# Kernel optimization log

Measured on AMD Instinct MI355X. Metric: run time of the kernel, lower is better.

Reference implementation:

```python
import jax, jax.numpy as jnp
import numpy as np


def _phi(x):
    # ELU(x) + 1 feature map (positive kernel feature map)
    return jax.nn.elu(x) + 1.0


def setup_inputs() -> dict:
    key = jax.random.key(0)
    k1, k2, k3 = jax.random.split(key, 3)
    B, S, E = 4, 4096, 1024
    inputs = jax.random.normal(k1, (B, S, E), dtype=jnp.float32)
    mask = jnp.ones((B, S), dtype=jnp.float32)
    w_qkv = jax.random.normal(k2, (3 * E, E), dtype=jnp.float32) * (E ** -0.5)
    b_qkv = jax.random.normal(k3, (3 * E,), dtype=jnp.float32) * 0.02
    return {"inputs": inputs, "mask": mask, "w_qkv": w_qkv, "b_qkv": b_qkv, "num_heads": 16}


def reference(inputs, mask, w_qkv, b_qkv, num_heads):
    B, S, E = inputs.shape
    H = num_heads
    D = E // H
    # qkv projection: torch Linear is x @ W.T + b
    qkv = inputs @ w_qkv.T + b_qkv                     # (B, S, 3E)
    qkv = qkv.reshape(B, S, 3, H, D)
    q = qkv[:, :, 0]                                   # (B, S, H, D)
    k = qkv[:, :, 1]
    v = qkv[:, :, 2]
    # key masking (float multiply, as in einsum 'bshd,bs->bshd')
    k = k * mask[:, :, None, None]
    kq = _phi(q)                                       # (B, S, H, D)
    kk = _phi(k)                                       # (B, S, H, D)
    # kv outer-product accumulation over sequence: (B, H, M, D)
    kv = jnp.einsum('bshd,bshm->bhmd', kk, v)
    # normalizer
    z = 1.0 / (jnp.einsum('bshd,bhd->bsh', kq, kk.sum(axis=1)) + 1e-6)
    # final contraction
    attn = jnp.einsum('bshd,bhmd,bsh->bshm', kq, kv, z)  # (B, S, H, D)
    attn = attn.reshape(B, S, E)
    # NOTE: original forward computes a projection but returns `attn` (dropout is
    # identity at inference), so projection is dead code and omitted here.
    return attn
```

## Files before the change

kernel.cpp:

```cpp
#include <hip/hip_runtime.h>

typedef unsigned short u16;
typedef short bf16x8 __attribute__((ext_vector_type(8)));
typedef float f32x4 __attribute__((ext_vector_type(4)));
typedef u16 u16x8 __attribute__((ext_vector_type(8)));
typedef u16 u16x4 __attribute__((ext_vector_type(4)));

#define B_ 4
#define S_ 4096
#define E_ 1024
#define H_ 16
#define D_ 64
#define M_ 16384
#define N_ 3072
#define K_ 1024

__device__ __forceinline__ u16 f2b(float f) {
    unsigned x = __builtin_bit_cast(unsigned, f);
    return (u16)((x + 0x7fffu + ((x >> 16) & 1u)) >> 16);
}
__device__ __forceinline__ float b2f(u16 u) {
    unsigned x = ((unsigned)u) << 16;
    return __builtin_bit_cast(float, x);
}
__device__ __forceinline__ float phi_f(float x) { return x > 0.f ? x + 1.f : __expf(x); }

__device__ __forceinline__ void gload16(const void* g, void* l) {
    __builtin_amdgcn_global_load_lds((const __attribute__((address_space(1))) void*)g,
                                     (__attribute__((address_space(3))) void*)l, 16, 0, 0);
}

#define MEMFENCE asm volatile("" ::: "memory")

__global__ void cvt_bf16(const float* __restrict__ in, u16* __restrict__ out, int n8) {
    int stride = gridDim.x * blockDim.x;
    for (int i = blockIdx.x * blockDim.x + threadIdx.x; i < n8; i += stride) {
        const float4* p = (const float4*)(in + (size_t)i * 8);
        float4 a = p[0], b = p[1];
        u16x8 o;
        o[0] = f2b(a.x); o[1] = f2b(a.y); o[2] = f2b(a.z); o[3] = f2b(a.w);
        o[4] = f2b(b.x); o[5] = f2b(b.y); o[6] = f2b(b.z); o[7] = f2b(b.w);
        *(u16x8*)(out + (size_t)i * 8) = o;
    }
}


__global__ __launch_bounds__(512, 2) void gemm_qkv(
    const u16* __restrict__ Abf, const u16* __restrict__ Wbf,
    const float* __restrict__ bias, const float* __restrict__ mask,
    u16* __restrict__ KQ, u16* __restrict__ KKT, u16* __restrict__ VT)
{
    __shared__ __align__(16) char lds[131072];

    int wg  = blockIdx.x;
    int xcd = wg & 7, ii = wg >> 3;
    int tm  = xcd * 8 + ii / 12;
    int tn  = ii % 12;
    int m0 = tm << 8, n0 = tn << 8;

    int t = threadIdx.x;
    int l = t & 63, wid = t >> 6;
    int wr = wid >> 2, wc = wid & 3;
    int lg = l >> 4, lr = l & 15;

    int srow  = t >> 3;
    int scolE = ((t & 7) ^ (srow & 7)) << 3;
    int t16   = t * 16;

    const u16* gA = Abf + (size_t)(m0 + srow) * K_ + scolE;
    const u16* gB = Wbf + (size_t)(n0 + srow) * K_ + scolE;

    const char* aB = lds + (wr * 128 + lr) * 128;
    const char* bB = lds + 32768 + (wc * 64 + lr) * 128;
    int pc0 = (lg * 16) ^ ((lr & 7) << 4);
    int pc1 = pc0 ^ 64;

    f32x4 acc[8][4] = {};
    bf16x8 av[4][2], b01[2][2], b23[2][2];

#define RD_A(BO, MI0) { _Pragma("unroll") for (int m_ = 0; m_ < 4; ++m_) { \
    av[m_][0] = *(const bf16x8*)(aB + (BO) + (MI0 + m_) * 2048 + pc0); \
    av[m_][1] = *(const bf16x8*)(aB + (BO) + (MI0 + m_) * 2048 + pc1); } }

#define RD_B01(BO) { _Pragma("unroll") for (int n_ = 0; n_ < 2; ++n_) { \
    b01[n_][0] = *(const bf16x8*)(bB + (BO) + n_ * 2048 + pc0); \
    b01[n_][1] = *(const bf16x8*)(bB + (BO) + n_ * 2048 + pc1); } }

#define RD_B23(BO) { _Pragma("unroll") for (int n_ = 0; n_ < 2; ++n_) { \
    b23[n_][0] = *(const bf16x8*)(bB + (BO) + (2 + n_) * 2048 + pc0); \
    b23[n_][1] = *(const bf16x8*)(bB + (BO) + (2 + n_) * 2048 + pc1); } }

#define ST_A(TT, HI, BO) { \
    gload16(gA + (size_t)((HI) * 64) * K_ + (TT) * 64, lds + (BO) + (HI) * 8192 + t16); \
    gload16(gA + (size_t)((HI) * 64 + 128) * K_ + (TT) * 64, lds + (BO) + 16384 + (HI) * 8192 + t16); }

#define ST_B(TT, PR, BO) { \
    gload16(gB + (size_t)((PR) * 128) * K_ + (TT) * 64, lds + (BO) + 32768 + (PR) * 16384 + t16); \
    gload16(gB + (size_t)((PR) * 128 + 64) * K_ + (TT) * 64, lds + (BO) + 32768 + (PR) * 16384 + 8192 + t16); }

#define BAR { MEMFENCE; __builtin_amdgcn_s_barrier(); MEMFENCE; }
#define LGKM0 { asm volatile("s_waitcnt lgkmcnt(0)" ::: "memory"); \
                __builtin_amdgcn_sched_barrier(0); }

#define MM16(MI0, NI0, BV) { __builtin_amdgcn_s_setprio(1); \
    _Pragma("unroll") for (int m_ = 0; m_ < 4; ++m_) \
    _Pragma("unroll") for (int n_ = 0; n_ < 2; ++n_) \
    _Pragma("unroll") for (int h_ = 0; h_ < 2; ++h_) \
        acc[(MI0) + m_][(NI0) + n_] = __builtin_amdgcn_mfma_f32_16x16x32_bf16( \
            av[m_][h_], BV[n_][h_], acc[(MI0) + m_][(NI0) + n_], 0, 0, 0); \
    __builtin_amdgcn_s_setprio(0); }

    ST_A(0, 0, 0); ST_B(0, 0, 0); ST_B(0, 1, 0); ST_A(0, 1, 0);
    ST_A(1, 0, 65536); ST_B(1, 0, 65536);
    asm volatile("s_waitcnt vmcnt(4)" ::: "memory");
    __builtin_amdgcn_s_barrier();
    MEMFENCE;

#pragma unroll 1
    for (int kt = 0; kt < 16; kt += 2) {
        int tp2 = kt + 2 < 16 ? kt + 2 : 15;
        int tp3 = kt + 3 < 16 ? kt + 3 : 15;
        RD_A(0, 0); RD_B01(0); ST_A(kt + 1, 1, 65536);
        BAR; LGKM0; MM16(0, 0, b01);
        RD_B23(0); ST_B(kt + 1, 1, 65536);
        BAR; LGKM0; MM16(0, 2, b23);
        RD_A(0, 4); ST_A(tp2, 0, 0);
        BAR; LGKM0; MM16(4, 2, b23);
        ST_B(tp2, 0, 0);
        asm volatile("s_waitcnt vmcnt(4)" ::: "memory");
        BAR; LGKM0; MM16(4, 0, b01);
        RD_A(65536, 0); RD_B01(65536); ST_A(tp2, 1, 0);
        BAR; LGKM0; MM16(0, 0, b01);
        RD_B23(65536); ST_B(tp2, 1, 0);
        BAR; LGKM0; MM16(0, 2, b23);
        RD_A(65536, 4); ST_A(tp3, 0, 65536);
        BAR; LGKM0; MM16(4, 2, b23);
        ST_B(tp3, 0, 65536);
        asm volatile("s_waitcnt vmcnt(4)" ::: "memory");
        BAR; LGKM0; MM16(4, 0, b01);
    }

    int part = n0 >> 10;

    float bv[4];
#pragma unroll
    for (int ni = 0; ni < 4; ++ni) bv[ni] = bias[n0 + wc * 64 + ni * 16 + lr];

    if (part == 0) {
#pragma unroll
        for (int mi = 0; mi < 8; ++mi)
#pragma unroll
            for (int j = 0; j < 4; ++j) {
                int row = m0 + wr * 128 + mi * 16 + lg * 4 + j;
#pragma unroll
                for (int ni = 0; ni < 4; ++ni) {
                    int col = n0 + wc * 64 + ni * 16 + lr;
                    KQ[(size_t)row * E_ + col] = f2b(phi_f(acc[mi][ni][j] + bv[ni]));
                }
            }
    } else {
        u16* dst0 = (part == 1) ? KKT : VT;
        int b  = m0 >> 12;
        int sl = m0 & (S_ - 1);
        int h  = ((tn & 3) << 2) | wc;
#pragma unroll
        for (int mi = 0; mi < 8; ++mi) {
            int sbase = sl + wr * 128 + mi * 16 + lg * 4;
            float mk[4];
#pragma unroll
            for (int j = 0; j < 4; ++j)
                mk[j] = (part == 1) ? mask[m0 + wr * 128 + mi * 16 + lg * 4 + j] : 1.f;
#pragma unroll
            for (int ni = 0; ni < 4; ++ni) {
                u16x4 o;
#pragma unroll
                for (int j = 0; j < 4; ++j) {
                    float v = acc[mi][ni][j] + bv[ni];
                    if (part == 1) v = phi_f(v * mk[j]);
                    o[j] = f2b(v);
                }
                int d = ni * 16 + lr;
                *(u16x4*)(dst0 + ((size_t)((b * H_ + h) * D_ + d)) * S_ + sbase) = o;
            }
        }
    }
}

__global__ __launch_bounds__(256) void kv_ksum_partial(
    const u16* __restrict__ VT, const u16* __restrict__ KKT,
    float* __restrict__ KVP, float* __restrict__ KSP)
{
    __shared__ __align__(16) u16 smem[8192];
    u16* As = smem;
    u16* Bs = smem + 4096;
    int bh = blockIdx.x;
    int ch = blockIdx.y;
    int s0 = ch << 8;
    int t = threadIdx.x;
    int l = t & 63, w = t >> 6;
    int lg = l >> 4, lr = l & 15;
    const u16* Ag = VT + (size_t)bh * (D_ * S_);
    const u16* Bg = KKT + (size_t)bh * (D_ * S_);
    int srow = t >> 3, scol = (t & 7) << 3;

    f32x4 acc[4] = {};
    float ks = 0.f;
    int kd = t >> 2;
    int kq4 = (t & 3) << 4;

    for (int kt = 0; kt < 4; ++kt) {
        __syncthreads();
        int sb = s0 + kt * 64;
#pragma unroll
        for (int i = 0; i < 2; ++i) {
            gload16(Ag + (size_t)(srow + i * 32) * S_ + sb + scol, As + i * 2048 + t * 8);
            gload16(Bg + (size_t)(srow + i * 32) * S_ + sb + scol, Bs + i * 2048 + t * 8);
        }
        __syncthreads();
#pragma unroll
        for (int i = 0; i < 16; ++i) ks += b2f(Bs[kd * 64 + kq4 + i]);
#pragma unroll
        for (int kh = 0; kh < 2; ++kh) {
            int ko = kh * 32 + lg * 8;
            bf16x8 a = *(const bf16x8*)&As[(w * 16 + lr) * 64 + ko];
#pragma unroll
            for (int ni = 0; ni < 4; ++ni) {
                bf16x8 bb = *(const bf16x8*)&Bs[(ni * 16 + lr) * 64 + ko];
                acc[ni] = __builtin_amdgcn_mfma_f32_16x16x32_bf16(a, bb, acc[ni], 0, 0, 0);
            }
        }
    }
    float* kvp = KVP + (size_t)ch * (64 * 4096) + bh * 4096;
#pragma unroll
    for (int ni = 0; ni < 4; ++ni)
#pragma unroll
        for (int j = 0; j < 4; ++j)
            kvp[(w * 16 + lg * 4 + j) * 64 + ni * 16 + lr] = acc[ni][j];
    ks += __shfl_xor(ks, 1);
    ks += __shfl_xor(ks, 2);
    if ((t & 3) == 0) KSP[ch * 4096 + bh * 64 + kd] = ks;
}

__global__ void reduce_kv(const float* __restrict__ KVP, const float* __restrict__ KSP,
                          float* __restrict__ KV, float* __restrict__ KSUM)
{
    int g = blockIdx.x * 256 + threadIdx.x;
#pragma unroll 1
    for (int i = g * 4; i < g * 4 + 4; ++i) {
        float s = 0.f;
#pragma unroll
        for (int c = 0; c < 16; ++c) s += KVP[(size_t)c * (64 * 4096) + i];
        KV[i] = s;
    }
    if (g < 4096) {
        float s = 0.f;
#pragma unroll
        for (int c = 0; c < 16; ++c) s += KSP[c * 4096 + g];
        KSUM[g] = s;
    }
}

__global__ __launch_bounds__(256) void attn_out(
    const u16* __restrict__ KQ, const float* __restrict__ KV,
    const float* __restrict__ KSUM, float* __restrict__ Out)
{
    __shared__ __align__(16) u16 kqs[16384];
    __shared__ __align__(16) u16 bsm[5120];
    __shared__ float den[256];
    int bh = blockIdx.x, ch = blockIdx.y;
    int b = bh >> 4, h = bh & 15;
    int t = threadIdx.x;
    int l = t & 63, w = t >> 6;
    int lg = l >> 4, lr = l & 15;
    size_t row0 = (size_t)b * S_ + ch * 256;
    int srow = t >> 3, scol = (t & 7) << 3;
#pragma unroll
    for (int i = 0; i < 8; ++i)
        gload16(KQ + (row0 + srow + i * 32) * E_ + h * 64 + scol, kqs + i * 2048 + t * 8);

    const float* kvg = KV + bh * 4096;
#pragma unroll
    for (int ii = 0; ii < 16; ii += 4) {
        float4 v = *(const float4*)(kvg + t * 16 + ii);
        u16x4 o; o[0] = f2b(v.x); o[1] = f2b(v.y); o[2] = f2b(v.z); o[3] = f2b(v.w);
        *(u16x4*)&bsm[t * 16 + ii] = o;
    }
    if (t < 64) bsm[4096 + t] = f2b(KSUM[bh * 64 + t]);
    for (int i = t; i < 960; i += 256) bsm[4160 + i] = 0;
    __syncthreads();

    f32x4 acc[4][5] = {};
#pragma unroll
    for (int kh = 0; kh < 2; ++kh) {
        int ko = kh * 32 + lg * 8;
        bf16x8 af[4];
#pragma unroll
        for (int mi = 0; mi < 4; ++mi)
            af[mi] = *(const bf16x8*)&kqs[(w * 64 + mi * 16 + lr) * 64 + ko];
#pragma unroll
        for (int ni = 0; ni < 5; ++ni) {
            bf16x8 bb = *(const bf16x8*)&bsm[(ni * 16 + lr) * 64 + ko];
#pragma unroll
            for (int mi = 0; mi < 4; ++mi)
                acc[mi][ni] = __builtin_amdgcn_mfma_f32_16x16x32_bf16(af[mi], bb, acc[mi][ni], 0, 0, 0);
        }
    }
    if (lr == 0) {
#pragma unroll
        for (int mi = 0; mi < 4; ++mi)
#pragma unroll
            for (int j = 0; j < 4; ++j)
                den[w * 64 + mi * 16 + lg * 4 + j] = acc[mi][4][j];
    }
    __syncthreads();
#pragma unroll
    for (int mi = 0; mi < 4; ++mi)
#pragma unroll
        for (int j = 0; j < 4; ++j) {
            int sl = w * 64 + mi * 16 + lg * 4 + j;
            float z = 1.f / (den[sl] + 1e-6f);
            float* op = Out + (row0 + sl) * E_ + h * 64;
#pragma unroll
            for (int ni = 0; ni < 4; ++ni)
                op[ni * 16 + lr] = acc[mi][ni][j] * z;
        }
}

extern "C" void kernel_launch(void* const* d_in, const int* in_sizes, int n_in,
                              void* d_out, int out_size, void* d_ws, size_t ws_size,
                              hipStream_t stream)
{
    const float* inputs = (const float*)d_in[0];
    const float* mask   = (const float*)d_in[1];
    const float* w_qkv  = (const float*)d_in[2];
    const float* b_qkv  = (const float*)d_in[3];

    u16* Abf = (u16*)d_ws;
    u16* Wbf = Abf + (size_t)M_ * K_;
    u16* KQ  = Wbf + (size_t)N_ * K_;
    float* KVP  = (float*)(KQ + (size_t)M_ * E_);
    float* KSP  = KVP + 16 * 64 * 4096;
    float* KV   = KSP + 16 * 4096;
    float* KSUM = KV + 64 * 4096;

    u16* KKT = (u16*)d_out;
    u16* VT  = KKT + (size_t)M_ * E_;

    cvt_bf16<<<2048, 256, 0, stream>>>(inputs, Abf, M_ * K_ / 8);
    cvt_bf16<<<768, 256, 0, stream>>>(w_qkv, Wbf, N_ * K_ / 8);
    gemm_qkv<<<768, 512, 0, stream>>>(Abf, Wbf, b_qkv, mask, KQ, KKT, VT);
    kv_ksum_partial<<<dim3(64, 16), 256, 0, stream>>>(VT, KKT, KVP, KSP);
    reduce_kv<<<256, 256, 0, stream>>>(KVP, KSP, KV, KSUM);
    attn_out<<<dim3(64, 16), 256, 0, stream>>>(KQ, KV, KSUM, (float*)d_out);
}
```

Measured before the change: 171.9 us.

## Fuse KV/ksum partial reduction into QKV GEMM, keeping phi(K) in LDS

Each workgroup now computes the V, K and Q tiles for one 256-row block and four heads in sequence. The phi(K) tile is written transposed into LDS instead of to global memory, and the V^T·phi(K) partial product and the key-sum partial are computed in the same kernel. This removes the separate kv_ksum_partial launch and the global round trip of the K^T buffer. In exchange the grid shrinks from 768 to 256 workgroups of three serial tiles each, which lowers parallelism on a machine with many CUs. V is also re-read from global memory immediately after it is written.

```diff
diff --git a/kernel.cpp b/kernel.cpp
--- a/kernel.cpp
+++ b/kernel.cpp
@@ -31,6 +31,10 @@
 }
 
 #define MEMFENCE asm volatile("" ::: "memory")
+#define BAR { MEMFENCE; __builtin_amdgcn_s_barrier(); MEMFENCE; }
+#define LGKM0 { asm volatile("s_waitcnt lgkmcnt(0)" ::: "memory"); \
+                __builtin_amdgcn_sched_barrier(0); }
+#define VMCNT(n) asm volatile("s_waitcnt vmcnt(" #n ")" ::: "memory")
 
 __global__ void cvt_bf16(const float* __restrict__ in, u16* __restrict__ out, int n8) {
     int stride = gridDim.x * blockDim.x;
@@ -45,39 +49,6 @@
 }
 
 
-__global__ __launch_bounds__(512, 2) void gemm_qkv(
-    const u16* __restrict__ Abf, const u16* __restrict__ Wbf,
-    const float* __restrict__ bias, const float* __restrict__ mask,
-    u16* __restrict__ KQ, u16* __restrict__ KKT, u16* __restrict__ VT)
-{
-    __shared__ __align__(16) char lds[131072];
-
-    int wg  = blockIdx.x;
-    int xcd = wg & 7, ii = wg >> 3;
-    int tm  = xcd * 8 + ii / 12;
-    int tn  = ii % 12;
-    int m0 = tm << 8, n0 = tn << 8;
-
-    int t = threadIdx.x;
-    int l = t & 63, wid = t >> 6;
-    int wr = wid >> 2, wc = wid & 3;
-    int lg = l >> 4, lr = l & 15;
-
-    int srow  = t >> 3;
-    int scolE = ((t & 7) ^ (srow & 7)) << 3;
-    int t16   = t * 16;
-
-    const u16* gA = Abf + (size_t)(m0 + srow) * K_ + scolE;
-    const u16* gB = Wbf + (size_t)(n0 + srow) * K_ + scolE;
-
-    const char* aB = lds + (wr * 128 + lr) * 128;
-    const char* bB = lds + 32768 + (wc * 64 + lr) * 128;
-    int pc0 = (lg * 16) ^ ((lr & 7) << 4);
-    int pc1 = pc0 ^ 64;
-
-    f32x4 acc[8][4] = {};
-    bf16x8 av[4][2], b01[2][2], b23[2][2];
-
 #define RD_A(BO, MI0) { _Pragma("unroll") for (int m_ = 0; m_ < 4; ++m_) { \
     av[m_][0] = *(const bf16x8*)(aB + (BO) + (MI0 + m_) * 2048 + pc0); \
     av[m_][1] = *(const bf16x8*)(aB + (BO) + (MI0 + m_) * 2048 + pc1); } }
@@ -97,10 +68,6 @@
 #define ST_B(TT, PR, BO) { \
     gload16(gB + (size_t)((PR) * 128) * K_ + (TT) * 64, lds + (BO) + 32768 + (PR) * 16384 + t16); \
     gload16(gB + (size_t)((PR) * 128 + 64) * K_ + (TT) * 64, lds + (BO) + 32768 + (PR) * 16384 + 8192 + t16); }
-
-#define BAR { MEMFENCE; __builtin_amdgcn_s_barrier(); MEMFENCE; }
-#define LGKM0 { asm volatile("s_waitcnt lgkmcnt(0)" ::: "memory"); \
-                __builtin_amdgcn_sched_barrier(0); }
 
 #define MM16(MI0, NI0, BV) { __builtin_amdgcn_s_setprio(1); \
     _Pragma("unroll") for (int m_ = 0; m_ < 4; ++m_) \
@@ -110,43 +77,165 @@
             av[m_][h_], BV[n_][h_], acc[(MI0) + m_][(NI0) + n_], 0, 0, 0); \
     __builtin_amdgcn_s_setprio(0); }
 
+__device__ __forceinline__ void run_tile(
+    const u16* gA, const u16* gB, char* lds, int t16,
+    const char* aB, const char* bB, int pc0, int pc1, f32x4 (&acc)[8][4])
+{
+    bf16x8 av[4][2], b01[2][2], b23[2][2];
     ST_A(0, 0, 0); ST_B(0, 0, 0); ST_B(0, 1, 0); ST_A(0, 1, 0);
     ST_A(1, 0, 65536); ST_B(1, 0, 65536);
-    asm volatile("s_waitcnt vmcnt(4)" ::: "memory");
+    VMCNT(4);
     __builtin_amdgcn_s_barrier();
     MEMFENCE;
-
 #pragma unroll 1
     for (int kt = 0; kt < 16; kt += 2) {
         int tp2 = kt + 2 < 16 ? kt + 2 : 15;
         int tp3 = kt + 3 < 16 ? kt + 3 : 15;
-        RD_A(0, 0); RD_B01(0); ST_A(kt + 1, 1, 65536);
-        BAR; LGKM0; MM16(0, 0, b01);
-        RD_B23(0); ST_B(kt + 1, 1, 65536);
-        BAR; LGKM0; MM16(0, 2, b23);
-        RD_A(0, 4); ST_A(tp2, 0, 0);
-        BAR; LGKM0; MM16(4, 2, b23);
-        ST_B(tp2, 0, 0);
-        asm volatile("s_waitcnt vmcnt(4)" ::: "memory");
-        BAR; LGKM0; MM16(4, 0, b01);
-        RD_A(65536, 0); RD_B01(65536); ST_A(tp2, 1, 0);
-        BAR; LGKM0; MM16(0, 0, b01);
-        RD_B23(65536); ST_B(tp2, 1, 0);
-        BAR; LGKM0; MM16(0, 2, b23);
-        RD_A(65536, 4); ST_A(tp3, 0, 65536);
-        BAR; LGKM0; MM16(4, 2, b23);
-        ST_B(tp3, 0, 65536);
-        asm volatile("s_waitcnt vmcnt(4)" ::: "memory");
-        BAR; LGKM0; MM16(4, 0, b01);
-    }
-
-    int part = n0 >> 10;
-
-    float bv[4];
-#pragma unroll
-    for (int ni = 0; ni < 4; ++ni) bv[ni] = bias[n0 + wc * 64 + ni * 16 + lr];
-
-    if (part == 0) {
+        RD_A(0, 0); RD_B01(0); ST_A(kt + 1, 1, 65536); BAR; LGKM0; MM16(0, 0, b01);
+        RD_B23(0);  ST_B(kt + 1, 1, 65536);            BAR; LGKM0; MM16(0, 2, b23);
+        RD_A(0, 4); ST_A(tp2, 0, 0);                   BAR; LGKM0; MM16(4, 2, b23);
+        ST_B(tp2, 0, 0); VMCNT(4);                     BAR; LGKM0; MM16(4, 0, b01);
+        RD_A(65536, 0); RD_B01(65536); ST_A(tp2, 1, 0); BAR; LGKM0; MM16(0, 0, b01);
+        RD_B23(65536);  ST_B(tp2, 1, 0);                BAR; LGKM0; MM16(0, 2, b23);
+        RD_A(65536, 4); ST_A(tp3, 0, 65536);            BAR; LGKM0; MM16(4, 2, b23);
+        ST_B(tp3, 0, 65536); VMCNT(4);                  BAR; LGKM0; MM16(4, 0, b01);
+    }
+    VMCNT(0);
+    __builtin_amdgcn_s_barrier();
+    MEMFENCE;
+}
+
+__global__ __launch_bounds__(512, 2) void gemm_fused(
+    const u16* __restrict__ Abf, const u16* __restrict__ Wbf,
+    const float* __restrict__ bias, const float* __restrict__ mask,
+    u16* __restrict__ KQ, u16* VT,
+    float* __restrict__ KVP, float* __restrict__ KSP)
+{
+    __shared__ __align__(16) char lds[131072];
+
+    int wg  = blockIdx.x;
+    int xcd = wg & 7, ii = wg >> 3;
+    int tm  = xcd * 8 + (ii >> 2);
+    int g   = ii & 3;
+    int m0  = tm << 8;
+    int b   = tm >> 4;
+    int s0  = (tm & 15) << 8;
+
+    int t = threadIdx.x;
+    int l = t & 63, wid = t >> 6;
+    int wr = wid >> 2, wc = wid & 3;
+    int lg = l >> 4, lr = l & 15;
+
+    int srow  = t >> 3;
+    int scolE = ((t & 7) ^ (srow & 7)) << 3;
+    int t16   = t * 16;
+
+    const u16* gA = Abf + (size_t)(m0 + srow) * K_ + scolE;
+    const char* aB = lds + (wr * 128 + lr) * 128;
+    const char* bB = lds + 32768 + (wc * 64 + lr) * 128;
+    int pc0 = (lg * 16) ^ ((lr & 7) << 4);
+    int pc1 = pc0 ^ 64;
+
+    {
+        int n0 = 2048 + g * 256;
+        const u16* gB = Wbf + (size_t)(n0 + srow) * K_ + scolE;
+        f32x4 acc[8][4] = {};
+        run_tile(gA, gB, lds, t16, aB, bB, pc0, pc1, acc);
+        float bv[4];
+#pragma unroll
+        for (int ni = 0; ni < 4; ++ni) bv[ni] = bias[n0 + wc * 64 + ni * 16 + lr];
+        int h = g * 4 + wc;
+#pragma unroll
+        for (int mi = 0; mi < 8; ++mi) {
+            int sbase = s0 + wr * 128 + mi * 16 + lg * 4;
+#pragma unroll
+            for (int ni = 0; ni < 4; ++ni) {
+                u16x4 o;
+#pragma unroll
+                for (int j = 0; j < 4; ++j) o[j] = f2b(acc[mi][ni][j] + bv[ni]);
+                int d = ni * 16 + lr;
+                *(u16x4*)(VT + ((size_t)((b * H_ + h) * D_ + d)) * S_ + sbase) = o;
+            }
+        }
+    }
+
+    {
+        int n0 = 1024 + g * 256;
+        const u16* gB = Wbf + (size_t)(n0 + srow) * K_ + scolE;
+        f32x4 acc[8][4] = {};
+        run_tile(gA, gB, lds, t16, aB, bB, pc0, pc1, acc);
+        float bv[4];
+#pragma unroll
+        for (int ni = 0; ni < 4; ++ni) bv[ni] = bias[n0 + wc * 64 + ni * 16 + lr];
+#pragma unroll
+        for (int mi = 0; mi < 8; ++mi) {
+            int sl0 = wr * 128 + mi * 16 + lg * 4;
+            float mk[4];
+#pragma unroll
+            for (int j = 0; j < 4; ++j) mk[j] = mask[m0 + sl0 + j];
+#pragma unroll
+            for (int ni = 0; ni < 4; ++ni) {
+                int d = ni * 16 + lr;
+                u16x4 o;
+#pragma unroll
+                for (int j = 0; j < 4; ++j)
+                    o[j] = f2b(phi_f((acc[mi][ni][j] + bv[ni]) * mk[j]));
+                *(u16x4*)(lds + wc * 32768 + d * 512 + ((sl0 * 2) ^ ((d & 7) << 4))) = o;
+            }
+        }
+    }
+    __syncthreads();
+
+    {
+        int head = wid & 3, mh = wid >> 2;
+        int bh = b * 16 + g * 4 + head;
+        f32x4 akv[2][4] = {};
+        const u16* vbase = VT + ((size_t)(bh * 64 + mh * 32 + lr)) * S_ + s0;
+#pragma unroll
+        for (int ks = 0; ks < 8; ++ks) {
+            bf16x8 vf[2];
+#pragma unroll
+            for (int mi = 0; mi < 2; ++mi)
+                vf[mi] = *(const bf16x8*)(vbase + (size_t)mi * 16 * S_ + ks * 32 + lg * 8);
+#pragma unroll
+            for (int ni = 0; ni < 4; ++ni) {
+                int dd = ni * 16 + lr;
+                bf16x8 kf = *(const bf16x8*)(lds + head * 32768 + dd * 512 +
+                                             ((ks * 64 + lg * 16) ^ ((dd & 7) << 4)));
+                akv[0][ni] = __builtin_amdgcn_mfma_f32_16x16x32_bf16(vf[0], kf, akv[0][ni], 0, 0, 0);
+                akv[1][ni] = __builtin_amdgcn_mfma_f32_16x16x32_bf16(vf[1], kf, akv[1][ni], 0, 0, 0);
+            }
+        }
+        float* kvp = KVP + ((size_t)(tm & 15) * 64 + bh) * 4096;
+#pragma unroll
+        for (int mi = 0; mi < 2; ++mi)
+#pragma unroll
+            for (int ni = 0; ni < 4; ++ni)
+#pragma unroll
+                for (int j = 0; j < 4; ++j)
+                    kvp[(mh * 32 + mi * 16 + lg * 4 + j) * 64 + ni * 16 + lr] = akv[mi][ni][j];
+        int hd = t >> 7, dd2 = (t >> 1) & 63, hf = t & 1;
+        float ksm = 0.f;
+#pragma unroll
+        for (int i = 0; i < 16; ++i) {
+            bf16x8 kk8 = *(const bf16x8*)(lds + hd * 32768 + dd2 * 512 +
+                                          ((hf * 256 + i * 16) ^ ((dd2 & 7) << 4)));
+#pragma unroll
+            for (int e = 0; e < 8; ++e) ksm += b2f((u16)kk8[e]);
+        }
+        ksm += __shfl_xor(ksm, 1);
+        if (!hf) KSP[(tm & 15) * 4096 + (b * 16 + g * 4 + hd) * 64 + dd2] = ksm;
+    }
+    __syncthreads();
+
+    {
+        int n0 = g * 256;
+        const u16* gB = Wbf + (size_t)(n0 + srow) * K_ + scolE;
+        f32x4 acc[8][4] = {};
+        run_tile(gA, gB, lds, t16, aB, bB, pc0, pc1, acc);
+        float bv[4];
+#pragma unroll
+        for (int ni = 0; ni < 4; ++ni) bv[ni] = bias[n0 + wc * 64 + ni * 16 + lr];
 #pragma unroll
         for (int mi = 0; mi < 8; ++mi)
 #pragma unroll
@@ -158,87 +247,7 @@
                     KQ[(size_t)row * E_ + col] = f2b(phi_f(acc[mi][ni][j] + bv[ni]));
                 }
             }
-    } else {
-        u16* dst0 = (part == 1) ? KKT : VT;
-        int b  = m0 >> 12;
-        int sl = m0 & (S_ - 1);
-        int h  = ((tn & 3) << 2) | wc;
-#pragma unroll
-        for (int mi = 0; mi < 8; ++mi) {
-            int sbase = sl + wr * 128 + mi * 16 + lg * 4;
-            float mk[4];
-#pragma unroll
-            for (int j = 0; j < 4; ++j)
-                mk[j] = (part == 1) ? mask[m0 + wr * 128 + mi * 16 + lg * 4 + j] : 1.f;
-#pragma unroll
-            for (int ni = 0; ni < 4; ++ni) {
-                u16x4 o;
-#pragma unroll
-                for (int j = 0; j < 4; ++j) {
-                    float v = acc[mi][ni][j] + bv[ni];
-                    if (part == 1) v = phi_f(v * mk[j]);
-                    o[j] = f2b(v);
-                }
-                int d = ni * 16 + lr;
-                *(u16x4*)(dst0 + ((size_t)((b * H_ + h) * D_ + d)) * S_ + sbase) = o;
-            }
-        }
-    }
-}
-
-__global__ __launch_bounds__(256) void kv_ksum_partial(
-    const u16* __restrict__ VT, const u16* __restrict__ KKT,
-    float* __restrict__ KVP, float* __restrict__ KSP)
-{
-    __shared__ __align__(16) u16 smem[8192];
-    u16* As = smem;
-    u16* Bs = smem + 4096;
-    int bh = blockIdx.x;
-    int ch = blockIdx.y;
-    int s0 = ch << 8;
-    int t = threadIdx.x;
-    int l = t & 63, w = t >> 6;
-    int lg = l >> 4, lr = l & 15;
-    const u16* Ag = VT + (size_t)bh * (D_ * S_);
-    const u16* Bg = KKT + (size_t)bh * (D_ * S_);
-    int srow = t >> 3, scol = (t & 7) << 3;
-
-    f32x4 acc[4] = {};
-    float ks = 0.f;
-    int kd = t >> 2;
-    int kq4 = (t & 3) << 4;
-
-    for (int kt = 0; kt < 4; ++kt) {
-        __syncthreads();
-        int sb = s0 + kt * 64;
-#pragma unroll
-        for (int i = 0; i < 2; ++i) {
-            gload16(Ag + (size_t)(srow + i * 32) * S_ + sb + scol, As + i * 2048 + t * 8);
-            gload16(Bg + (size_t)(srow + i * 32) * S_ + sb + scol, Bs + i * 2048 + t * 8);
-        }
-        __syncthreads();
-#pragma unroll
-        for (int i = 0; i < 16; ++i) ks += b2f(Bs[kd * 64 + kq4 + i]);
-#pragma unroll
-        for (int kh = 0; kh < 2; ++kh) {
-            int ko = kh * 32 + lg * 8;
-            bf16x8 a = *(const bf16x8*)&As[(w * 16 + lr) * 64 + ko];
-#pragma unroll
-            for (int ni = 0; ni < 4; ++ni) {
-                bf16x8 bb = *(const bf16x8*)&Bs[(ni * 16 + lr) * 64 + ko];
-                acc[ni] = __builtin_amdgcn_mfma_f32_16x16x32_bf16(a, bb, acc[ni], 0, 0, 0);
-            }
-        }
-    }
-    float* kvp = KVP + (size_t)ch * (64 * 4096) + bh * 4096;
-#pragma unroll
-    for (int ni = 0; ni < 4; ++ni)
-#pragma unroll
-        for (int j = 0; j < 4; ++j)
-            kvp[(w * 16 + lg * 4 + j) * 64 + ni * 16 + lr] = acc[ni][j];
-    ks += __shfl_xor(ks, 1);
-    ks += __shfl_xor(ks, 2);
-    if ((t & 3) == 0) KSP[ch * 4096 + bh * 64 + kd] = ks;
+    }
 }
 
 __global__ void reduce_kv(const float* __restrict__ KVP, const float* __restrict__ KSP,
@@ -343,13 +352,11 @@
     float* KV   = KSP + 16 * 4096;
     float* KSUM = KV + 64 * 4096;
 
-    u16* KKT = (u16*)d_out;
-    u16* VT  = KKT + (size_t)M_ * E_;
+    u16* VT = (u16*)d_out;
 
     cvt_bf16<<<2048, 256, 0, stream>>>(inputs, Abf, M_ * K_ / 8);
     cvt_bf16<<<768, 256, 0, stream>>>(w_qkv, Wbf, N_ * K_ / 8);
-    gemm_qkv<<<768, 512, 0, stream>>>(Abf, Wbf, b_qkv, mask, KQ, KKT, VT);
-    kv_ksum_partial<<<dim3(64, 16), 256, 0, stream>>>(VT, KKT, KVP, KSP);
+    gemm_fused<<<256, 512, 0, stream>>>(Abf, Wbf, b_qkv, mask, KQ, VT, KVP, KSP);
     reduce_kv<<<256, 256, 0, stream>>>(KVP, KSP, KV, KSUM);
     attn_out<<<dim3(64, 16), 256, 0, stream>>>(KQ, KV, KSUM, (float*)d_out);
 }
```

Measured after the change: 156.2 us. 1.1x faster.
